# Performance work log

Measured on AMD Instinct MI355X. Metric: run time of the kernel, lower is better.

The kernel has to match this reference:

```python
import jax, jax.numpy as jnp
import numpy as np

NUM_GROUPS = 6
K = 40
CODEBOOK = 1024
VQ_COMMIT = 0.25


def setup_inputs() -> dict:
    key = jax.random.key(0)
    k1, k2 = jax.random.split(key)
    z = jax.random.normal(k1, (32, 60, 8000), dtype=jnp.float32)
    embeddings = jax.random.normal(k2, (NUM_GROUPS, K, CODEBOOK), dtype=jnp.float32)
    return {"z": z, "embeddings": embeddings}


def reference(z, embeddings):
    # z: (N, 60, T) -> reshape to (N, 240, T//4) as in Group_Quantize.forward
    N, C, T = z.shape
    z2 = z.reshape(N, C * 4, -1)          # (N, 240, Tp)
    Tp = z2.shape[-1]
    # split into groups and move channel last (EMAQuantizer transposes 1,-1)
    x = z2.reshape(N, NUM_GROUPS, K, Tp)
    x = jnp.transpose(x, (1, 0, 3, 2))    # (G, N, Tp, K)
    flat = x.reshape(NUM_GROUPS, N * Tp, K)  # (G, R, K)

    dist = (jnp.sum(flat ** 2, axis=-1, keepdims=True)
            - 2.0 * jnp.einsum('grk,gkc->grc', flat, embeddings)
            + jnp.sum(embeddings ** 2, axis=1)[:, None, :])  # (G, R, C)
    idx = jnp.argmin(dist, axis=-1)       # (G, R)

    # codebook lookup per group (embedding stored as (K, C), code vectors are columns)
    quant = jax.vmap(lambda e, i: jnp.take(e.T, i, axis=0))(embeddings, idx)  # (G, R, K)

    x4 = x                                 # (G, N, Tp, K)
    q4 = quant.reshape(NUM_GROUPS, N, Tp, K)

    # commitment loss per group, per batch element
    diff = VQ_COMMIT * jnp.mean((jax.lax.stop_gradient(q4) - x4) ** 2, axis=(2, 3))  # (G, N)
    vq_loss = jnp.sum(diff, axis=0) / NUM_GROUPS  # (N,)

    # straight-through estimator
    q_ste = x4 + jax.lax.stop_gradient(q4 - x4)   # (G, N, Tp, K)
    q_merge = jnp.transpose(q_ste, (1, 0, 3, 2)).reshape(N, NUM_GROUPS * K, Tp)  # (N, 240, Tp)
    q_merge = q_merge.reshape(N, (NUM_GROUPS * K) // 4, -1)  # (N, 60, T)
    return q_merge, vq_loss
```

## Files before the change

kernel.cpp:

```cpp
#include <hip/hip_runtime.h>
#include <math.h>

#define NG 6
#define KD 40
#define CB 1024
#define NB 32
#define TP 2000
#define RPB 128
#define THREADS 256
#define NBLK 500
#define ZN 480000
#define ZG 80000
#define BAND_D 6e-3f
#define PK_G 98304
#define PK_T 3072
#define CHS 6144
#define NCH 16

typedef __attribute__((ext_vector_type(8))) short bf16x8;
typedef __attribute__((ext_vector_type(16))) float f32x16;

__device__ __forceinline__ unsigned short bf16rne(float v) {
  unsigned u = __float_as_uint(v);
  return (unsigned short)((u + 0x7FFFu + ((u >> 16) & 1u)) >> 16);
}
__device__ __forceinline__ float bf16val(unsigned short h) {
  return __uint_as_float(((unsigned)h) << 16);
}
__device__ __forceinline__ void bf16split(float v, unsigned short& h, unsigned short& l) {
  h = bf16rne(v);
  l = bf16rne(v - bf16val(h));
}
__device__ __forceinline__ bf16x8 ldfrag16(const unsigned short* p) {
  union { uint4 q; bf16x8 v; } u;
  u.q = *(const uint4*)p;
  return u.v;
}
__device__ __forceinline__ void gload_lds16(const void* g, void* l) {
  __builtin_amdgcn_global_load_lds(
      (const __attribute__((address_space(1))) unsigned int*)g,
      (__attribute__((address_space(3))) unsigned int*)l, 16, 0, 0);
}

__global__ void prep_kernel(const float* __restrict__ emb, float* __restrict__ et,
                            float* __restrict__ e2, unsigned short* __restrict__ epack) {
  int c = blockIdx.x * blockDim.x + threadIdx.x;
  int g = blockIdx.y;
  if (c >= CB) return;
  const float* eg = emb + (size_t)g * KD * CB;
  float ev[KD];
  float* o = et + ((size_t)g * CB + c) * KD;
  float s = 0.f;
#pragma unroll
  for (int k = 0; k < KD; ++k) {
    float v = eg[k * CB + c];
    ev[k] = v;
    o[k] = v;
    s = __fadd_rn(s, __fmul_rn(v, v));
  }
  e2[g * CB + c] = s;

  float sv = 0.5f * s;
  unsigned short p0 = bf16rne(sv);
  float v1 = sv - bf16val(p0);
  unsigned short p1 = bf16rne(v1);
  unsigned short p2 = bf16rne(v1 - bf16val(p1));

  int tile = c >> 5, j32 = c & 31;
  unsigned short* tb = epack + (size_t)g * PK_G + (size_t)tile * PK_T;
#pragma unroll
  for (int s2 = 0; s2 < 3; ++s2)
#pragma unroll
    for (int gg = 0; gg < 2; ++gg) {
      union { uint4 q; unsigned short sh[8]; } uh, ul;
#pragma unroll
      for (int j = 0; j < 8; ++j) {
        int k = s2 * 16 + gg * 8 + j;
        if (k < KD) {
          bf16split(ev[k], uh.sh[j], ul.sh[j]);
        } else {
          uh.sh[j] = (k == 40) ? p0 : (k == 41) ? p1 : (k == 42) ? p2 : (unsigned short)0;
          ul.sh[j] = 0;
        }
      }
      unsigned short* ph = tb + ((size_t)(s2 * 2 + gg) * 32 + j32) * 8;
      *(uint4*)ph = uh.q;
      *(uint4*)(ph + 1536) = ul.q;
    }
}

__device__ __forceinline__ float npd_calc(const float* __restrict__ x,
                                          const float* __restrict__ ef,
                                          float e2c, float x2np) {
  float dot = 0.f;
#pragma unroll
  for (int k = 0; k < KD; ++k) dot = __fadd_rn(dot, __fmul_rn(x[k], ef[k]));
  return __fadd_rn(__fsub_rn(x2np, __fadd_rn(dot, dot)), e2c);
}

__global__ __launch_bounds__(THREADS, 4) void vq_kernel(
    const float* __restrict__ z, const float* __restrict__ et,
    const float* __restrict__ e2, const unsigned short* __restrict__ epack,
    float* __restrict__ out, float* __restrict__ partials) {
  const int g = blockIdx.y;
  const int bb = blockIdx.x;
  const int tid = threadIdx.x;
  const int lane = tid & 63;
  const int gg = lane >> 5;
  const int j32 = lane & 31;
  const int wid = tid >> 6;
  const int rowloc = wid * 32 + j32;
  const int rid = bb * RPB + rowloc;
  const int n = rid / TP;
  const int tt = rid - n * TP;

  const float* etg = et + (size_t)g * CB * KD;
  const float* e2g = e2 + g * CB;
  const unsigned short* egrp = epack + (size_t)g * PK_G;

  __shared__ __align__(16) unsigned short sbuf[2][CHS];
  __shared__ float r0s[THREADS], r1s[THREADS];

#define STAGE(B, CH) { \
    const unsigned short* gsrc = egrp + (size_t)(CH) * CHS + wid * 512 + lane * 8; \
    unsigned short* lb = &sbuf[B][wid * 512]; \
    gload_lds16(gsrc, lb); \
    gload_lds16(gsrc + 2048, lb + 2048); \
    gload_lds16(gsrc + 4096, lb + 4096); }
  STAGE(0, 0)

  const float* zp = z + (size_t)n * ZN + (size_t)g * ZG + tt;
  float x[KD];
#pragma unroll
  for (int k = 0; k < KD; ++k) x[k] = zp[(size_t)k * TP];
  float x2np;
  {
    float r[8];
#pragma unroll
    for (int j = 0; j < 8; ++j) r[j] = __fmul_rn(x[j], x[j]);
#pragma unroll
    for (int i = 8; i < KD; i += 8)
#pragma unroll
      for (int j = 0; j < 8; ++j)
        r[j] = __fadd_rn(r[j], __fmul_rn(x[i + j], x[i + j]));
    x2np = __fadd_rn(__fadd_rn(__fadd_rn(r[0], r[1]), __fadd_rn(r[2], r[3])),
                     __fadd_rn(__fadd_rn(r[4], r[5]), __fadd_rn(r[6], r[7])));
  }

  bf16x8 xh[3], xl[3];
#define PACK8(DH, DL, B0) { \
    union { unsigned short s[8]; bf16x8 v; } uh, ul; \
    _Pragma("unroll") \
    for (int j = 0; j < 8; ++j) { \
      unsigned short h, l; bf16split(-x[(B0) + j], h, l); \
      uh.s[j] = h; ul.s[j] = l; } \
    DH = uh.v; DL = ul.v; }
  if (gg == 0) {
    PACK8(xh[0], xl[0], 0)
    PACK8(xh[1], xl[1], 16)
    PACK8(xh[2], xl[2], 32)
  } else {
    PACK8(xh[0], xl[0], 8)
    PACK8(xh[1], xl[1], 24)
    union { unsigned short s[8]; bf16x8 v; } uh;
#pragma unroll
    for (int j = 0; j < 8; ++j) uh.s[j] = (j < 3) ? (unsigned short)0x3F80 : (unsigned short)0;
    xh[2] = uh.v;
    union { unsigned short s[8]; bf16x8 v; } uz;
#pragma unroll
    for (int j = 0; j < 8; ++j) uz.s[j] = 0;
    xl[2] = uz.v;
  }
#undef PACK8

  f32x16 zacc;
#pragma unroll
  for (int i = 0; i < 16; ++i) zacc[i] = 0.f;

  float d1 = INFINITY, d2 = INFINITY, d3 = INFINITY;
  int i1 = 0, i2 = 0, i3 = 0;

#define INS3(V, C) { \
    bool u1 = (V) < d1, u2 = (V) < d2, u3 = (V) < d3; \
    d3 = u2 ? d2 : (u3 ? (V) : d3); i3 = u2 ? i2 : (u3 ? (C) : i3); \
    d2 = u1 ? d1 : (u2 ? (V) : d2); i2 = u1 ? i1 : (u2 ? (C) : i2); \
    d1 = u1 ? (V) : d1;             i1 = u1 ? (C) : i1; }

#define TRACK(AV, TILE) { \
    float gm0 = fminf(fminf(AV[0], AV[1]), fminf(AV[2], AV[3])); \
    float gm1 = fminf(fminf(AV[4], AV[5]), fminf(AV[6], AV[7])); \
    float gm2 = fminf(fminf(AV[8], AV[9]), fminf(AV[10], AV[11])); \
    float gm3 = fminf(fminf(AV[12], AV[13]), fminf(AV[14], AV[15])); \
    float tmin = fminf(fminf(gm0, gm1), fminf(gm2, gm3)); \
    if (tmin < d3) { \
      int cb = (TILE) * 32 + 4 * gg; \
      if (gm0 < d3) { INS3(AV[0], cb + 0) INS3(AV[1], cb + 1) INS3(AV[2], cb + 2) INS3(AV[3], cb + 3) } \
      if (gm1 < d3) { INS3(AV[4], cb + 8) INS3(AV[5], cb + 9) INS3(AV[6], cb + 10) INS3(AV[7], cb + 11) } \
      if (gm2 < d3) { INS3(AV[8], cb + 16) INS3(AV[9], cb + 17) INS3(AV[10], cb + 18) INS3(AV[11], cb + 19) } \
      if (gm3 < d3) { INS3(AV[12], cb + 24) INS3(AV[13], cb + 25) INS3(AV[14], cb + 26) INS3(AV[15], cb + 27) } \
    } }

#define COMPUTE_TILE(T2, TILE) { \
    const unsigned short* tb = &sbuf[cur][(T2) * PK_T + lane * 8]; \
    bf16x8 eh0 = ldfrag16(tb); \
    bf16x8 eh1 = ldfrag16(tb + 512); \
    bf16x8 eh2 = ldfrag16(tb + 1024); \
    bf16x8 el0 = ldfrag16(tb + 1536); \
    bf16x8 el1 = ldfrag16(tb + 2048); \
    bf16x8 el2 = ldfrag16(tb + 2560); \
    f32x16 a; \
    a = __builtin_amdgcn_mfma_f32_32x32x16_bf16(eh0, xh[0], zacc, 0, 0, 0); \
    a = __builtin_amdgcn_mfma_f32_32x32x16_bf16(eh0, xl[0], a, 0, 0, 0); \
    a = __builtin_amdgcn_mfma_f32_32x32x16_bf16(el0, xh[0], a, 0, 0, 0); \
    a = __builtin_amdgcn_mfma_f32_32x32x16_bf16(eh1, xh[1], a, 0, 0, 0); \
    a = __builtin_amdgcn_mfma_f32_32x32x16_bf16(eh1, xl[1], a, 0, 0, 0); \
    a = __builtin_amdgcn_mfma_f32_32x32x16_bf16(el1, xh[1], a, 0, 0, 0); \
    a = __builtin_amdgcn_mfma_f32_32x32x16_bf16(eh2, xh[2], a, 0, 0, 0); \
    a = __builtin_amdgcn_mfma_f32_32x32x16_bf16(eh2, xl[2], a, 0, 0, 0); \
    a = __builtin_amdgcn_mfma_f32_32x32x16_bf16(el2, xh[2], a, 0, 0, 0); \
    TRACK(a, TILE) }

  int cur = 0;
#pragma unroll 1
  for (int ch = 0; ch < NCH; ++ch) {
    if (ch + 1 < NCH) {
      STAGE(cur ^ 1, ch + 1)
      asm volatile("s_waitcnt vmcnt(3)" ::: "memory");
    } else {
      asm volatile("s_waitcnt vmcnt(0)" ::: "memory");
    }
    __builtin_amdgcn_s_barrier();
    COMPUTE_TILE(0, ch * 2)
    COMPUTE_TILE(1, ch * 2 + 1)
    __builtin_amdgcn_s_barrier();
    cur ^= 1;
  }

  float dd1 = fmaf(2.f, d1, x2np);
  float dd2 = fmaf(2.f, d2, x2np);
  float dd3 = fmaf(2.f, d3, x2np);
  float bd = dd1;
  int bi = i1;
  bool exact = false;
  {
    bool need2 = dd2 < dd1 + BAND_D;
    bool need3 = dd3 < dd1 + BAND_D;
    if (need2 || need3) {
      int cA = i1;
      int cB = need2 ? i2 : 0x7fffffff;
      int cC = need3 ? i3 : 0x7fffffff;
      int t;
      if (cA > cB) { t = cA; cA = cB; cB = t; }
      if (cB > cC) { t = cB; cB = cC; cC = t; }
      if (cA > cB) { t = cA; cA = cB; cB = t; }
      bd = INFINITY; bi = CB;
      if (cA < CB) { float d = npd_calc(x, etg + (size_t)cA * KD, e2g[cA], x2np); if (d < bd) { bd = d; bi = cA; } }
      if (cB < CB) { float d = npd_calc(x, etg + (size_t)cB * KD, e2g[cB], x2np); if (d < bd) { bd = d; bi = cB; } }
      if (cC < CB) { float d = npd_calc(x, etg + (size_t)cC * KD, e2g[cC], x2np); if (d < bd) { bd = d; bi = cC; } }
      exact = true;
    }
  }
  {
    float od = __shfl_xor(bd, 32);
    bool race = fabsf(bd - od) < BAND_D;
    if (race && !exact) bd = npd_calc(x, etg + (size_t)bi * KD, e2g[bi], x2np);
    float od2 = __shfl_xor(bd, 32);
    int oi = __shfl_xor(bi, 32);
    if (od2 < bd || (od2 == bd && oi < bi)) { bd = od2; bi = oi; }
  }

  const float4* eb4 = (const float4*)(etg + (size_t)bi * KD);
  float* op = out + (size_t)n * ZN + (size_t)g * ZG + tt;
  float ls = 0.f;
  if (gg == 0) {
#pragma unroll
    for (int p = 0; p < 5; ++p) {
      float4 v = eb4[p];
      int k = 4 * p;
      float e0 = __fsub_rn(v.x, x[k + 0]); ls = fmaf(e0, e0, ls); op[(size_t)(k + 0) * TP] = __fadd_rn(x[k + 0], e0);
      float e1 = __fsub_rn(v.y, x[k + 1]); ls = fmaf(e1, e1, ls); op[(size_t)(k + 1) * TP] = __fadd_rn(x[k + 1], e1);
      float e2v = __fsub_rn(v.z, x[k + 2]); ls = fmaf(e2v, e2v, ls); op[(size_t)(k + 2) * TP] = __fadd_rn(x[k + 2], e2v);
      float e3 = __fsub_rn(v.w, x[k + 3]); ls = fmaf(e3, e3, ls); op[(size_t)(k + 3) * TP] = __fadd_rn(x[k + 3], e3);
    }
  } else {
#pragma unroll
    for (int p = 5; p < 10; ++p) {
      float4 v = eb4[p];
      int k = 4 * p;
      float e0 = __fsub_rn(v.x, x[k + 0]); ls = fmaf(e0, e0, ls); op[(size_t)(k + 0) * TP] = __fadd_rn(x[k + 0], e0);
      float e1 = __fsub_rn(v.y, x[k + 1]); ls = fmaf(e1, e1, ls); op[(size_t)(k + 1) * TP] = __fadd_rn(x[k + 1], e1);
      float e2v = __fsub_rn(v.z, x[k + 2]); ls = fmaf(e2v, e2v, ls); op[(size_t)(k + 2) * TP] = __fadd_rn(x[k + 2], e2v);
      float e3 = __fsub_rn(v.w, x[k + 3]); ls = fmaf(e3, e3, ls); op[(size_t)(k + 3) * TP] = __fadd_rn(x[k + 3], e3);
    }
  }

  const int n_lo = (bb * RPB) / TP;
  r0s[tid] = (n == n_lo) ? ls : 0.f;
  r1s[tid] = (n == n_lo) ? 0.f : ls;
  __syncthreads();
  for (int s = THREADS / 2; s > 0; s >>= 1) {
    if (tid < s) {
      r0s[tid] += r0s[tid + s];
      r1s[tid] += r1s[tid + s];
    }
    __syncthreads();
  }
  if (tid == 0) {
    partials[((size_t)g * NBLK + bb) * 2 + 0] = r0s[0];
    partials[((size_t)g * NBLK + bb) * 2 + 1] = r1s[0];
  }
}

__global__ void loss_kernel(const float* __restrict__ partials,
                            float* __restrict__ vq) {
  int n = threadIdx.x;
  if (n >= NB) return;
  float acc = 0.f;
  for (int g = 0; g < NG; ++g) {
    float s = 0.f;
    int b0 = (n * TP) / RPB;
    int b1 = ((n + 1) * TP - 1) / RPB;
    for (int b = b0; b <= b1; ++b) {
      int n_lo = (b * RPB) / TP;
      s += partials[((size_t)g * NBLK + b) * 2 + ((n == n_lo) ? 0 : 1)];
    }
    acc += 0.25f * (s / 80000.0f);
  }
  vq[n] = acc / 6.0f;
}

extern "C" void kernel_launch(void* const* d_in, const int* in_sizes, int n_in,
                              void* d_out, int out_size, void* d_ws, size_t ws_size,
                              hipStream_t stream) {
  const float* z = (const float*)d_in[0];
  const float* emb = (const float*)d_in[1];
  float* out = (float*)d_out;

  float* et = (float*)d_ws;
  float* e2 = et + (size_t)NG * CB * KD;
  float* partials = e2 + (size_t)NG * CB;
  unsigned short* epack = (unsigned short*)((char*)d_ws + 1031680);

  prep_kernel<<<dim3(CB / 256, NG), 256, 0, stream>>>(emb, et, e2, epack);
  vq_kernel<<<dim3(NBLK, NG), THREADS, 0, stream>>>(z, et, e2, epack, out, partials);
  loss_kernel<<<1, 64, 0, stream>>>(partials, out + (size_t)NB * 60 * 8000);
}
```

Measured before the change: 222.8 us.

## Track per-group minima in main loop, rescan codebook only for near-ties

```diff
diff --git a/kernel.cpp b/kernel.cpp
--- a/kernel.cpp
+++ b/kernel.cpp
@@ -177,48 +177,36 @@
 #pragma unroll
   for (int i = 0; i < 16; ++i) zacc[i] = 0.f;
 
-  float d1 = INFINITY, d2 = INFINITY, d3 = INFINITY;
-  int i1 = 0, i2 = 0, i3 = 0;
-
-#define INS3(V, C) { \
-    bool u1 = (V) < d1, u2 = (V) < d2, u3 = (V) < d3; \
-    d3 = u2 ? d2 : (u3 ? (V) : d3); i3 = u2 ? i2 : (u3 ? (C) : i3); \
-    d2 = u1 ? d1 : (u2 ? (V) : d2); i2 = u1 ? i1 : (u2 ? (C) : i2); \
-    d1 = u1 ? (V) : d1;             i1 = u1 ? (C) : i1; }
-
-#define TRACK(AV, TILE) { \
-    float gm0 = fminf(fminf(AV[0], AV[1]), fminf(AV[2], AV[3])); \
-    float gm1 = fminf(fminf(AV[4], AV[5]), fminf(AV[6], AV[7])); \
-    float gm2 = fminf(fminf(AV[8], AV[9]), fminf(AV[10], AV[11])); \
-    float gm3 = fminf(fminf(AV[12], AV[13]), fminf(AV[14], AV[15])); \
-    float tmin = fminf(fminf(gm0, gm1), fminf(gm2, gm3)); \
-    if (tmin < d3) { \
-      int cb = (TILE) * 32 + 4 * gg; \
-      if (gm0 < d3) { INS3(AV[0], cb + 0) INS3(AV[1], cb + 1) INS3(AV[2], cb + 2) INS3(AV[3], cb + 3) } \
-      if (gm1 < d3) { INS3(AV[4], cb + 8) INS3(AV[5], cb + 9) INS3(AV[6], cb + 10) INS3(AV[7], cb + 11) } \
-      if (gm2 < d3) { INS3(AV[8], cb + 16) INS3(AV[9], cb + 17) INS3(AV[10], cb + 18) INS3(AV[11], cb + 19) } \
-      if (gm3 < d3) { INS3(AV[12], cb + 24) INS3(AV[13], cb + 25) INS3(AV[14], cb + 26) INS3(AV[15], cb + 27) } \
-    } }
-
-#define COMPUTE_TILE(T2, TILE) { \
-    const unsigned short* tb = &sbuf[cur][(T2) * PK_T + lane * 8]; \
-    bf16x8 eh0 = ldfrag16(tb); \
-    bf16x8 eh1 = ldfrag16(tb + 512); \
-    bf16x8 eh2 = ldfrag16(tb + 1024); \
-    bf16x8 el0 = ldfrag16(tb + 1536); \
-    bf16x8 el1 = ldfrag16(tb + 2048); \
-    bf16x8 el2 = ldfrag16(tb + 2560); \
-    f32x16 a; \
-    a = __builtin_amdgcn_mfma_f32_32x32x16_bf16(eh0, xh[0], zacc, 0, 0, 0); \
-    a = __builtin_amdgcn_mfma_f32_32x32x16_bf16(eh0, xl[0], a, 0, 0, 0); \
-    a = __builtin_amdgcn_mfma_f32_32x32x16_bf16(el0, xh[0], a, 0, 0, 0); \
-    a = __builtin_amdgcn_mfma_f32_32x32x16_bf16(eh1, xh[1], a, 0, 0, 0); \
-    a = __builtin_amdgcn_mfma_f32_32x32x16_bf16(eh1, xl[1], a, 0, 0, 0); \
-    a = __builtin_amdgcn_mfma_f32_32x32x16_bf16(el1, xh[1], a, 0, 0, 0); \
-    a = __builtin_amdgcn_mfma_f32_32x32x16_bf16(eh2, xh[2], a, 0, 0, 0); \
-    a = __builtin_amdgcn_mfma_f32_32x32x16_bf16(eh2, xl[2], a, 0, 0, 0); \
-    a = __builtin_amdgcn_mfma_f32_32x32x16_bf16(el2, xh[2], a, 0, 0, 0); \
-    TRACK(a, TILE) }
+  float d1 = INFINITY, d2x = INFINITY;
+  int grp1 = 0;
+
+#define TRACKG(AV, TILE) { \
+    int cb = (TILE) * 32 + 4 * gg; \
+    float g0 = fminf(fminf(fminf(AV[0], AV[1]), AV[2]), AV[3]); \
+    float g1 = fminf(fminf(fminf(AV[4], AV[5]), AV[6]), AV[7]); \
+    float g2 = fminf(fminf(fminf(AV[8], AV[9]), AV[10]), AV[11]); \
+    float g3 = fminf(fminf(fminf(AV[12], AV[13]), AV[14]), AV[15]); \
+    d2x = fminf(d2x, fmaxf(d1, g0)); grp1 = (g0 < d1) ? (cb + 0) : grp1; d1 = fminf(d1, g0); \
+    d2x = fminf(d2x, fmaxf(d1, g1)); grp1 = (g1 < d1) ? (cb + 8) : grp1; d1 = fminf(d1, g1); \
+    d2x = fminf(d2x, fmaxf(d1, g2)); grp1 = (g2 < d1) ? (cb + 16) : grp1; d1 = fminf(d1, g2); \
+    d2x = fminf(d2x, fmaxf(d1, g3)); grp1 = (g3 < d1) ? (cb + 24) : grp1; d1 = fminf(d1, g3); }
+
+#define MFMA9(TB, AOUT) { \
+    bf16x8 eh0 = ldfrag16(TB); \
+    bf16x8 eh1 = ldfrag16((TB) + 512); \
+    bf16x8 eh2 = ldfrag16((TB) + 1024); \
+    bf16x8 el0 = ldfrag16((TB) + 1536); \
+    bf16x8 el1 = ldfrag16((TB) + 2048); \
+    bf16x8 el2 = ldfrag16((TB) + 2560); \
+    AOUT = __builtin_amdgcn_mfma_f32_32x32x16_bf16(eh0, xh[0], zacc, 0, 0, 0); \
+    AOUT = __builtin_amdgcn_mfma_f32_32x32x16_bf16(eh0, xl[0], AOUT, 0, 0, 0); \
+    AOUT = __builtin_amdgcn_mfma_f32_32x32x16_bf16(el0, xh[0], AOUT, 0, 0, 0); \
+    AOUT = __builtin_amdgcn_mfma_f32_32x32x16_bf16(eh1, xh[1], AOUT, 0, 0, 0); \
+    AOUT = __builtin_amdgcn_mfma_f32_32x32x16_bf16(eh1, xl[1], AOUT, 0, 0, 0); \
+    AOUT = __builtin_amdgcn_mfma_f32_32x32x16_bf16(el1, xh[1], AOUT, 0, 0, 0); \
+    AOUT = __builtin_amdgcn_mfma_f32_32x32x16_bf16(eh2, xh[2], AOUT, 0, 0, 0); \
+    AOUT = __builtin_amdgcn_mfma_f32_32x32x16_bf16(eh2, xl[2], AOUT, 0, 0, 0); \
+    AOUT = __builtin_amdgcn_mfma_f32_32x32x16_bf16(el2, xh[2], AOUT, 0, 0, 0); }
 
   int cur = 0;
 #pragma unroll 1
@@ -230,43 +218,98 @@
       asm volatile("s_waitcnt vmcnt(0)" ::: "memory");
     }
     __builtin_amdgcn_s_barrier();
-    COMPUTE_TILE(0, ch * 2)
-    COMPUTE_TILE(1, ch * 2 + 1)
+    {
+      const unsigned short* tb0 = &sbuf[cur][lane * 8];
+      f32x16 a0;
+      MFMA9(tb0, a0)
+      TRACKG(a0, ch * 2)
+      const unsigned short* tb1 = &sbuf[cur][PK_T + lane * 8];
+      f32x16 a1;
+      MFMA9(tb1, a1)
+      TRACKG(a1, ch * 2 + 1)
+    }
     __builtin_amdgcn_s_barrier();
     cur ^= 1;
   }
 
-  float dd1 = fmaf(2.f, d1, x2np);
-  float dd2 = fmaf(2.f, d2, x2np);
-  float dd3 = fmaf(2.f, d3, x2np);
-  float bd = dd1;
-  int bi = i1;
-  bool exact = false;
-  {
-    bool need2 = dd2 < dd1 + BAND_D;
-    bool need3 = dd3 < dd1 + BAND_D;
-    if (need2 || need3) {
-      int cA = i1;
-      int cB = need2 ? i2 : 0x7fffffff;
-      int cC = need3 ? i3 : 0x7fffffff;
-      int t;
-      if (cA > cB) { t = cA; cA = cB; cB = t; }
-      if (cB > cC) { t = cB; cB = cC; cC = t; }
-      if (cA > cB) { t = cA; cA = cB; cB = t; }
-      bd = INFINITY; bi = CB;
-      if (cA < CB) { float d = npd_calc(x, etg + (size_t)cA * KD, e2g[cA], x2np); if (d < bd) { bd = d; bi = cA; } }
-      if (cB < CB) { float d = npd_calc(x, etg + (size_t)cB * KD, e2g[cB], x2np); if (d < bd) { bd = d; bi = cB; } }
-      if (cC < CB) { float d = npd_calc(x, etg + (size_t)cC * KD, e2g[cC], x2np); if (d < bd) { bd = d; bi = cC; } }
-      exact = true;
-    }
-  }
+  float bd = INFINITY;
+  int bi = CB;
+#pragma unroll
+  for (int j = 0; j < 4; ++j) {
+    int c = grp1 + j;
+    float d = npd_calc(x, etg + (size_t)c * KD, e2g[c], x2np);
+    if (d < bd) { bd = d; bi = c; }
+  }
+  float dd2x = fmaf(2.f, d2x, x2np);
+
   {
     float od = __shfl_xor(bd, 32);
-    bool race = fabsf(bd - od) < BAND_D;
-    if (race && !exact) bd = npd_calc(x, etg + (size_t)bi * KD, e2g[bi], x2np);
-    float od2 = __shfl_xor(bd, 32);
     int oi = __shfl_xor(bi, 32);
-    if (od2 < bd || (od2 == bd && oi < bi)) { bd = od2; bi = oi; }
+    float odd2x = __shfl_xor(dd2x, 32);
+    if (od < bd || (od == bd && oi < bi)) { bd = od; bi = oi; }
+    dd2x = fminf(dd2x, odd2x);
+  }
+  bool flag = dd2x < bd + BAND_D;
+
+  if (__any(flag)) {
+    float rd1 = INFINITY, rd2 = INFINITY, rd3 = INFINITY;
+    int ri1 = 0, ri2 = 0, ri3 = 0;
+#define INS3(V, C) { \
+      bool u1 = (V) < rd1, u2 = (V) < rd2, u3 = (V) < rd3; \
+      rd3 = u2 ? rd2 : (u3 ? (V) : rd3); ri3 = u2 ? ri2 : (u3 ? (C) : ri3); \
+      rd2 = u1 ? rd1 : (u2 ? (V) : rd2); ri2 = u1 ? ri1 : (u2 ? (C) : ri2); \
+      rd1 = u1 ? (V) : rd1;              ri1 = u1 ? (C) : ri1; }
+#pragma unroll 1
+    for (int tile = 0; tile < 32; ++tile) {
+      const unsigned short* tb = egrp + (size_t)tile * PK_T + lane * 8;
+      f32x16 a;
+      MFMA9(tb, a)
+      {
+        float gm0 = fminf(fminf(a[0], a[1]), fminf(a[2], a[3]));
+        float gm1 = fminf(fminf(a[4], a[5]), fminf(a[6], a[7]));
+        float gm2 = fminf(fminf(a[8], a[9]), fminf(a[10], a[11]));
+        float gm3 = fminf(fminf(a[12], a[13]), fminf(a[14], a[15]));
+        float tmin = fminf(fminf(gm0, gm1), fminf(gm2, gm3));
+        if (tmin < rd3) {
+          int cb = tile * 32 + 4 * gg;
+          if (gm0 < rd3) { INS3(a[0], cb + 0) INS3(a[1], cb + 1) INS3(a[2], cb + 2) INS3(a[3], cb + 3) }
+          if (gm1 < rd3) { INS3(a[4], cb + 8) INS3(a[5], cb + 9) INS3(a[6], cb + 10) INS3(a[7], cb + 11) }
+          if (gm2 < rd3) { INS3(a[8], cb + 16) INS3(a[9], cb + 17) INS3(a[10], cb + 18) INS3(a[11], cb + 19) }
+          if (gm3 < rd3) { INS3(a[12], cb + 24) INS3(a[13], cb + 25) INS3(a[14], cb + 26) INS3(a[15], cb + 27) }
+        }
+      }
+    }
+    float dd1 = fmaf(2.f, rd1, x2np);
+    float dd2 = fmaf(2.f, rd2, x2np);
+    float dd3 = fmaf(2.f, rd3, x2np);
+    bd = dd1; bi = ri1;
+    bool exact = false;
+    {
+      bool need2 = dd2 < dd1 + BAND_D;
+      bool need3 = dd3 < dd1 + BAND_D;
+      if (need2 || need3) {
+        int cA = ri1;
+        int cB = need2 ? ri2 : 0x7fffffff;
+        int cC = need3 ? ri3 : 0x7fffffff;
+        int t;
+        if (cA > cB) { t = cA; cA = cB; cB = t; }
+        if (cB > cC) { t = cB; cB = cC; cC = t; }
+        if (cA > cB) { t = cA; cA = cB; cB = t; }
+        bd = INFINITY; bi = CB;
+        if (cA < CB) { float d = npd_calc(x, etg + (size_t)cA * KD, e2g[cA], x2np); if (d < bd) { bd = d; bi = cA; } }
+        if (cB < CB) { float d = npd_calc(x, etg + (size_t)cB * KD, e2g[cB], x2np); if (d < bd) { bd = d; bi = cB; } }
+        if (cC < CB) { float d = npd_calc(x, etg + (size_t)cC * KD, e2g[cC], x2np); if (d < bd) { bd = d; bi = cC; } }
+        exact = true;
+      }
+    }
+    {
+      float od = __shfl_xor(bd, 32);
+      bool race = fabsf(bd - od) < BAND_D;
+      if (race && !exact) bd = npd_calc(x, etg + (size_t)bi * KD, e2g[bi], x2np);
+      float od2 = __shfl_xor(bd, 32);
+      int oi = __shfl_xor(bi, 32);
+      if (od2 < bd || (od2 == bd && oi < bi)) { bd = od2; bi = oi; }
+    }
   }
 
   const float4* eb4 = (const float4*)(etg + (size_t)bi * KD);
```

Result: faster. 205.6 us (-7.7%).
